# Kernel tuning notes

Measured on AMD Instinct MI355X. Metric: run time of the kernel, lower is better.

The kernel has to match this reference:

```python
import jax, jax.numpy as jnp
import numpy as np

NUM_LAYERS, E, H = 4, 256, 8
HD = E // H
EPS = 1e-5


def _layer_norm(x, g, b):
    m = jnp.mean(x, axis=-1, keepdims=True)
    v = jnp.mean((x - m) ** 2, axis=-1, keepdims=True)
    return (x - m) / jnp.sqrt(v + EPS) * g + b


def _embed_rotary(x, pos):
    # x: [B, L, E], pos: [B, L, E, 2] (cos, sin)
    x2 = jnp.stack([-x[..., 1::2], x[..., ::2]], axis=-1).reshape(x.shape)
    return x * pos[..., 0] + x2 * pos[..., 1]


def setup_inputs() -> dict:
    key = jax.random.key(0)
    ks = jax.random.split(key, 16)
    Lq, B, Lkv = 512, 4, 4096
    s = 0.02
    return {
        "query": jax.random.normal(ks[0], (Lq, B, E), jnp.float32),
        "value": jax.random.normal(ks[1], (Lkv, B, E), jnp.float32),
        "query_pos": jax.random.normal(ks[2], (B, Lq, E, 2), jnp.float32),
        "value_pos": jax.random.normal(ks[3], (B, Lkv, E, 2), jnp.float32),
        "Wqkv": jax.random.normal(ks[4], (NUM_LAYERS, 3 * E, E), jnp.float32) * s,
        "bqkv": jnp.zeros((NUM_LAYERS, 3 * E), jnp.float32),
        "Wo": jax.random.normal(ks[5], (NUM_LAYERS, E, E), jnp.float32) * s,
        "bo": jnp.zeros((NUM_LAYERS, E), jnp.float32),
        "ln1_g": jnp.ones((NUM_LAYERS, E), jnp.float32),
        "ln1_b": jnp.zeros((NUM_LAYERS, E), jnp.float32),
        "W1": jax.random.normal(ks[6], (NUM_LAYERS, E, E), jnp.float32) * s,
        "b1": jnp.zeros((NUM_LAYERS, E), jnp.float32),
        "W2": jax.random.normal(ks[7], (NUM_LAYERS, E, E), jnp.float32) * s,
        "b2": jnp.zeros((NUM_LAYERS, E), jnp.float32),
        "ln2_g": jnp.ones((NUM_LAYERS, E), jnp.float32),
        "ln2_b": jnp.zeros((NUM_LAYERS, E), jnp.float32),
    }


def reference(query, value, query_pos, value_pos, Wqkv, bqkv, Wo, bo,
              ln1_g, ln1_b, W1, b1, W2, b2, ln2_g, ln2_b):
    Lq, B, _ = query.shape
    Lkv = value.shape[0]
    scale = HD ** -0.5

    def step(q_in, p):
        Wqkv_l, bqkv_l, Wo_l, bo_l, g1, be1, W1_l, b1_l, W2_l, b2_l, g2, be2 = p
        Wq, Wk, Wv = jnp.split(Wqkv_l, 3, axis=0)
        bq, bk, bv = jnp.split(bqkv_l, 3, axis=0)
        q = (q_in @ Wq.T + bq) * scale              # [Lq, B, E] (scaled as torch MHA)
        k = value @ Wk.T + bk                        # [Lkv, B, E]
        v = value @ Wv.T + bv
        qb = _embed_rotary(q.swapaxes(0, 1), query_pos)   # [B, Lq, E]
        kb = _embed_rotary(k.swapaxes(0, 1), value_pos)   # [B, Lkv, E]
        vb = v.swapaxes(0, 1)
        qh = qb.reshape(B, Lq, H, HD).transpose(0, 2, 1, 3)    # [B, H, Lq, HD]
        kh = kb.reshape(B, Lkv, H, HD).transpose(0, 2, 1, 3)
        vh = vb.reshape(B, Lkv, H, HD).transpose(0, 2, 1, 3)
        attn = jax.nn.softmax(jnp.einsum('bhqd,bhkd->bhqk', qh, kh), axis=-1)
        o = jnp.einsum('bhqk,bhkd->bhqd', attn, vh)            # [B, H, Lq, HD]
        o = o.transpose(0, 2, 1, 3).reshape(B, Lq, E).swapaxes(0, 1)  # [Lq, B, E]
        x = _layer_norm(q_in + o @ Wo_l.T + bo_l, g1, be1)
        ff = jax.nn.relu(x @ W1_l.T + b1_l) @ W2_l.T + b2_l
        y = _layer_norm(x + ff, g2, be2)
        return y, y

    params = (Wqkv, bqkv, Wo, bo, ln1_g, ln1_b, W1, b1, W2, b2, ln2_g, ln2_b)
    _, ys = jax.lax.scan(step, query, params)
    return ys  # [num_layers, Lq, B, E] — stacked per-layer outputs
```

## Files before the change

kernel.cpp:

```cpp
#include <hip/hip_runtime.h>
#include <hip/hip_bf16.h>

typedef __attribute__((ext_vector_type(8))) short short8;
typedef __attribute__((ext_vector_type(4))) float float4v;
typedef __attribute__((ext_vector_type(4))) unsigned short ushort4v;

#define LQ 512
#define NB 4
#define LKV 4096
#define E 256
#define NH 8
#define HD 32
#define NLAYER 4
#define QSCALE 0.17677669529663687f
#define SPLITS 4
#define KSPAN (LKV / SPLITS)
#define QT 128
#define CK 128

__device__ __forceinline__ unsigned short f2bf(float f) {
    union { float f; unsigned int i; } x; x.f = f;
    unsigned int r = x.i + 0x7fffu + ((x.i >> 16) & 1u);
    return (unsigned short)(r >> 16);
}
__device__ __forceinline__ unsigned int pack2(float a, float b) {
    union { float f; unsigned int i; } xa, xb; xa.f = a; xb.f = b;
    unsigned int ra = xa.i + 0x7fffu + ((xa.i >> 16) & 1u);
    unsigned int rb = xb.i + 0x7fffu + ((xb.i >> 16) & 1u);
    return (ra >> 16) | (rb & 0xffff0000u);
}
__device__ __forceinline__ unsigned int pack2_rtz(float a, float b) {
    union { float f; unsigned int i; } xa, xb; xa.f = a; xb.f = b;
    return __builtin_amdgcn_perm(xb.i, xa.i, 0x07060302u);
}
__device__ __forceinline__ float bf2f(unsigned short u) {
    union { unsigned int i; float f; } x; x.i = ((unsigned int)u) << 16; return x.f;
}
__device__ __forceinline__ float4v mfma16(short8 a, short8 b, float4v c) {
    return __builtin_amdgcn_mfma_f32_16x16x32_bf16(a, b, c, 0, 0, 0);
}

__global__ void pack_k(const float* __restrict__ in, unsigned short* __restrict__ out) {
    long i = ((long)blockIdx.x * 256 + threadIdx.x) * 8;
    float4 a = *(const float4*)&in[i];
    float4 b = *(const float4*)&in[i + 4];
    uint4 v;
    v.x = pack2(a.x, a.y); v.y = pack2(a.z, a.w);
    v.z = pack2(b.x, b.y); v.w = pack2(b.z, b.w);
    *(uint4*)&out[i] = v;
}

__global__ void init_cur(const float* __restrict__ q, float* __restrict__ cur,
                         unsigned short* __restrict__ cur_bf) {
    int i = blockIdx.x * 256 + threadIdx.x;
    float v = q[i];
    cur[i] = v;
    cur_bf[i] = f2bf(v);
}

__global__ __launch_bounds__(256) void gemm_k(
        const unsigned short* __restrict__ A, const unsigned short* __restrict__ W,
        const float* __restrict__ bias, unsigned short* __restrict__ out_bf) {
    __shared__ unsigned short sA[32 * 264];
    __shared__ unsigned short sB[64 * 264];
    const int t = threadIdx.x;
    const int lane = t & 63, wave = t >> 6, quad = lane >> 4, lid = lane & 15;
    const int row0 = blockIdx.x * 32, col0 = blockIdx.y * 64;
    {
        int r = t >> 3, ks = (t & 7) * 32;
        const unsigned short* ap = A + (long)(row0 + r) * E + ks;
#pragma unroll
        for (int i = 0; i < 4; i++)
            *(uint4*)&sA[r * 264 + ks + i * 8] = *(const uint4*)(ap + i * 8);
    }
    {
        int r = t >> 2, ks = (t & 3) * 64;
        const unsigned short* wp = W + (long)(col0 + r) * E + ks;
#pragma unroll
        for (int i = 0; i < 8; i++)
            *(uint4*)&sB[r * 264 + ks + i * 8] = *(const uint4*)(wp + i * 8);
    }
    __syncthreads();
    float4v acc[2];
    acc[0] = (float4v){0.f, 0.f, 0.f, 0.f};
    acc[1] = (float4v){0.f, 0.f, 0.f, 0.f};
#pragma unroll
    for (int k0 = 0; k0 < E; k0 += 32) {
        short8 bf = *(const short8*)&sB[(wave * 16 + lid) * 264 + k0 + quad * 8];
        short8 af0 = *(const short8*)&sA[(lid) * 264 + k0 + quad * 8];
        short8 af1 = *(const short8*)&sA[(16 + lid) * 264 + k0 + quad * 8];
        acc[0] = mfma16(af0, bf, acc[0]);
        acc[1] = mfma16(af1, bf, acc[1]);
    }
#pragma unroll
    for (int mt = 0; mt < 2; mt++)
#pragma unroll
        for (int r = 0; r < 4; r++) {
            int grow = row0 + mt * 16 + quad * 4 + r;
            int gcol = col0 + wave * 16 + lid;
            float v = fmaxf(acc[mt][r] + bias[gcol], 0.f);
            out_bf[(long)grow * E + gcol] = f2bf(v);
        }
}

template <int COMBINE, int OUT2>
__global__ __launch_bounds__(256) void gemm_ln(
        const unsigned short* __restrict__ A,
        const float* __restrict__ Opart, const float* __restrict__ lp,
        const unsigned short* __restrict__ W, const float* __restrict__ bias,
        const float* __restrict__ res, const float* __restrict__ g,
        const float* __restrict__ bvec, float* __restrict__ outf,
        unsigned short* __restrict__ out_bf, float* __restrict__ outf2) {
    __shared__ unsigned short sA[16 * 264];
    __shared__ float lnS[4][16];
    __shared__ float lnQ[4][16];
    const int t = threadIdx.x;
    const int lane = t & 63, wave = t >> 6, quad = lane >> 4, lid = lane & 15;
    const int row0 = blockIdx.x * 16;
    {
        const int r = t >> 4, cseg = t & 15;
        if (COMBINE) {
            const int grow = row0 + r;
            const int seq = grow >> 2, b = grow & 3;
            const int h = cseg >> 1, dd = (cseg & 1) * 16;
            const int bh = b * 8 + h;
            float L = 0.f;
            float av[16];
#pragma unroll
            for (int j = 0; j < 16; j++) av[j] = 0.f;
#pragma unroll
            for (int s = 0; s < SPLITS; s++) {
                long rbase = (long)(s * 32 + bh) * 512 + seq;
                L += lp[rbase];
#pragma unroll
                for (int jj = 0; jj < 4; jj++) {
                    float4 p = *(const float4*)&Opart[rbase * 32 + dd + jj * 4];
                    av[jj * 4 + 0] += p.x; av[jj * 4 + 1] += p.y;
                    av[jj * 4 + 2] += p.z; av[jj * 4 + 3] += p.w;
                }
            }
            float inv = 1.f / L;
            uint4 u0, u1;
            u0.x = pack2(av[0] * inv, av[1] * inv);   u0.y = pack2(av[2] * inv, av[3] * inv);
            u0.z = pack2(av[4] * inv, av[5] * inv);   u0.w = pack2(av[6] * inv, av[7] * inv);
            u1.x = pack2(av[8] * inv, av[9] * inv);   u1.y = pack2(av[10] * inv, av[11] * inv);
            u1.z = pack2(av[12] * inv, av[13] * inv); u1.w = pack2(av[14] * inv, av[15] * inv);
            *(uint4*)&sA[r * 264 + cseg * 16] = u0;
            *(uint4*)&sA[r * 264 + cseg * 16 + 8] = u1;
        } else {
            const unsigned short* ap = A + (long)(row0 + r) * E + cseg * 16;
            *(uint4*)&sA[r * 264 + cseg * 16] = *(const uint4*)ap;
            *(uint4*)&sA[r * 264 + cseg * 16 + 8] = *(const uint4*)(ap + 8);
        }
    }
    __syncthreads();
    float4v acc[4];
#pragma unroll
    for (int nf = 0; nf < 4; nf++) acc[nf] = (float4v){0.f, 0.f, 0.f, 0.f};
#pragma unroll
    for (int k0 = 0; k0 < E; k0 += 32) {
        short8 af = *(const short8*)&sA[lid * 264 + k0 + quad * 8];
#pragma unroll
        for (int nf = 0; nf < 4; nf++) {
            short8 bf = *(const short8*)(W + (long)(wave * 64 + nf * 16 + lid) * E + k0 + quad * 8);
            acc[nf] = mfma16(af, bf, acc[nf]);
        }
    }
    float v[4][4];
    float sr[4], qr_[4];
#pragma unroll
    for (int r = 0; r < 4; r++) { sr[r] = 0.f; qr_[r] = 0.f; }
#pragma unroll
    for (int nf = 0; nf < 4; nf++) {
        int col = wave * 64 + nf * 16 + lid;
        float bcol = bias[col];
#pragma unroll
        for (int r = 0; r < 4; r++) {
            int grow = row0 + quad * 4 + r;
            float val = acc[nf][r] + bcol + res[(long)grow * E + col];
            v[nf][r] = val;
            sr[r] += val;
            qr_[r] += val * val;
        }
    }
#pragma unroll
    for (int r = 0; r < 4; r++) {
#pragma unroll
        for (int d = 1; d < 16; d <<= 1) {
            sr[r] += __shfl_xor(sr[r], d);
            qr_[r] += __shfl_xor(qr_[r], d);
        }
    }
    if (lid == 0) {
#pragma unroll
        for (int r = 0; r < 4; r++) {
            lnS[wave][quad * 4 + r] = sr[r];
            lnQ[wave][quad * 4 + r] = qr_[r];
        }
    }
    __syncthreads();
    float mean[4], rstd[4];
#pragma unroll
    for (int r = 0; r < 4; r++) {
        int row = quad * 4 + r;
        float S = lnS[0][row] + lnS[1][row] + lnS[2][row] + lnS[3][row];
        float Q = lnQ[0][row] + lnQ[1][row] + lnQ[2][row] + lnQ[3][row];
        float mu = S * (1.f / 256.f);
        float var = Q * (1.f / 256.f) - mu * mu;
        mean[r] = mu;
        rstd[r] = rsqrtf(var + 1e-5f);
    }
#pragma unroll
    for (int nf = 0; nf < 4; nf++) {
        int col = wave * 64 + nf * 16 + lid;
        float gc = g[col], bc = bvec[col];
#pragma unroll
        for (int r = 0; r < 4; r++) {
            int grow = row0 + quad * 4 + r;
            float xo = (v[nf][r] - mean[r]) * rstd[r] * gc + bc;
            outf[(long)grow * E + col] = xo;
            out_bf[(long)grow * E + col] = f2bf(xo);
            if (OUT2) outf2[(long)grow * E + col] = xo;
        }
    }
}

__global__ __launch_bounds__(256) void qkv_q(
        const unsigned short* __restrict__ A, const unsigned short* __restrict__ W,
        const float* __restrict__ bias, const unsigned short* __restrict__ pos,
        unsigned short* __restrict__ qout) {
    __shared__ unsigned short sA[32 * 40];
    __shared__ unsigned short sB[64 * 40];
    const int t = threadIdx.x;
    const int lane = t & 63, wave = t >> 6, quad = lane >> 4, lid = lane & 15;
    const int row0 = blockIdx.x * 32, col0 = blockIdx.y * 64;
    const int sr = t >> 2, sk = (t & 3) * 8;
    const unsigned short* ap = A + (long)(row0 + sr) * E + sk;
    const unsigned short* wp = W + (long)(col0 + sr) * E + sk;
    uint4 av, bv;
    if (t < 128) av = *(const uint4*)ap;
    bv = *(const uint4*)wp;
    float4v acc[2];
    acc[0] = (float4v){0.f, 0.f, 0.f, 0.f};
    acc[1] = (float4v){0.f, 0.f, 0.f, 0.f};
#pragma unroll
    for (int ki = 0; ki < 8; ki++) {
        __syncthreads();
        if (t < 128) *(uint4*)&sA[sr * 40 + sk] = av;
        *(uint4*)&sB[sr * 40 + sk] = bv;
        __syncthreads();
        if (ki < 7) {
            if (t < 128) av = *(const uint4*)(ap + (ki + 1) * 32);
            bv = *(const uint4*)(wp + (ki + 1) * 32);
        }
        short8 af0 = *(const short8*)&sA[lid * 40 + quad * 8];
        short8 af1 = *(const short8*)&sA[(16 + lid) * 40 + quad * 8];
        short8 bf = *(const short8*)&sB[(wave * 16 + lid) * 40 + quad * 8];
        acc[0] = mfma16(af0, bf, acc[0]);
        acc[1] = mfma16(af1, bf, acc[1]);
    }
#pragma unroll
    for (int mt = 0; mt < 2; mt++)
#pragma unroll
        for (int r = 0; r < 4; r++) {
            int grow = row0 + mt * 16 + quad * 4 + r;
            int gcol = col0 + wave * 16 + lid;
            float v = (acc[mt][r] + bias[gcol]) * QSCALE;
            int seq = grow >> 2, b = grow & 3;
            int c = gcol;
            unsigned int cs = *(const unsigned int*)&pos[(((long)b * LQ + seq) * E + c) * 2];
            float cv = bf2f((unsigned short)cs), sv = bf2f((unsigned short)(cs >> 16));
            float p = __shfl_xor(v, 1);
            float x2 = (c & 1) ? p : -p;
            float rv = v * cv + x2 * sv;
            qout[(((long)b * NH + (c >> 5)) * LQ + seq) * HD + (c & 31)] = f2bf(rv);
        }
}

__global__ __launch_bounds__(256) void qkv_kv(
        const unsigned short* __restrict__ A, const unsigned short* __restrict__ Wall,
        const float* __restrict__ ball, const unsigned short* __restrict__ pos,
        unsigned short* __restrict__ kall, unsigned short* __restrict__ vtall) {
    const int layer = blockIdx.z;
    const unsigned short* W = Wall + (long)layer * 768 * 256 + 256 * 256;
    const float* bias = ball + (long)layer * 768 + 256;
    unsigned short* kout = kall + (long)layer * 4194304;
    unsigned short* vtout = vtall + (long)layer * 4194304;
    __shared__ unsigned short sA[64 * 40];
    __shared__ unsigned short sB[64 * 40];
    const int t = threadIdx.x;
    const int lane = t & 63, wave = t >> 6, quad = lane >> 4, lid = lane & 15;
    const int wr = wave >> 1, wc = wave & 1;
    const int row0 = blockIdx.x * 64, col0 = blockIdx.y * 64;
    const int sr = t >> 2, sk = (t & 3) * 8;
    const unsigned short* ap = A + (long)(row0 + sr) * E + sk;
    const unsigned short* wp = W + (long)(col0 + sr) * E + sk;
    uint4 av = *(const uint4*)ap;
    uint4 bv = *(const uint4*)wp;
    float4v acc[2][2];
    for (int i = 0; i < 2; i++) for (int j = 0; j < 2; j++) acc[i][j] = (float4v){0.f, 0.f, 0.f, 0.f};
#pragma unroll
    for (int ki = 0; ki < 8; ki++) {
        __syncthreads();
        *(uint4*)&sA[sr * 40 + sk] = av;
        *(uint4*)&sB[sr * 40 + sk] = bv;
        __syncthreads();
        if (ki < 7) {
            av = *(const uint4*)(ap + (ki + 1) * 32);
            bv = *(const uint4*)(wp + (ki + 1) * 32);
        }
        short8 af0 = *(const short8*)&sA[(wr * 32 + lid) * 40 + quad * 8];
        short8 af1 = *(const short8*)&sA[(wr * 32 + 16 + lid) * 40 + quad * 8];
        short8 bf0 = *(const short8*)&sB[(wc * 32 + lid) * 40 + quad * 8];
        short8 bf1 = *(const short8*)&sB[(wc * 32 + 16 + lid) * 40 + quad * 8];
        acc[0][0] = mfma16(af0, bf0, acc[0][0]);
        acc[0][1] = mfma16(af0, bf1, acc[0][1]);
        acc[1][0] = mfma16(af1, bf0, acc[1][0]);
        acc[1][1] = mfma16(af1, bf1, acc[1][1]);
    }
#pragma unroll
    for (int mt = 0; mt < 2; mt++)
#pragma unroll
        for (int nt = 0; nt < 2; nt++)
#pragma unroll
            for (int r = 0; r < 4; r++) {
                int grow = row0 + wr * 32 + mt * 16 + quad * 4 + r;
                int gcol = col0 + wc * 32 + nt * 16 + lid;
                float v = acc[mt][nt][r] + bias[gcol];
                int seq = grow >> 2, b = grow & 3;
                if (gcol < E) {
                    int c = gcol;
                    unsigned int cs = *(const unsigned int*)&pos[(((long)b * LKV + seq) * E + c) * 2];
                    float cv = bf2f((unsigned short)cs), sv = bf2f((unsigned short)(cs >> 16));
                    float p = __shfl_xor(v, 1);
                    float x2 = (c & 1) ? p : -p;
                    float rv = v * cv + x2 * sv;
                    kout[(((long)b * NH + (c >> 5)) * LKV + seq) * HD + (c & 31)] = f2bf(rv);
                } else {
                    int c = gcol - E;
                    vtout[(((long)b * NH + (c >> 5)) * HD + (c & 31)) * (long)LKV + seq] = f2bf(v);
                }
            }
}

__global__ __launch_bounds__(256) void attn_k(
        const unsigned short* __restrict__ qb, const unsigned short* __restrict__ kb,
        const unsigned short* __restrict__ vtb, float* __restrict__ Opart,
        float* __restrict__ lpart) {
    __shared__ unsigned short sK[CK * 40];
    __shared__ unsigned short sVT[32 * 136];
    __shared__ unsigned short sPT[4 * CK * 36];
    const int t = threadIdx.x;
    const int lane = t & 63, wave = t >> 6, quad = lane >> 4, lid = lane & 15;
    const int qt0 = blockIdx.x * QT;
    const int bh = blockIdx.y;
    const int key0 = blockIdx.z * KSPAN;
    const unsigned short* kbase = kb + (long)bh * LKV * HD;
    const unsigned short* vbase = vtb + (long)bh * HD * LKV;
    short8 aq[2];
#pragma unroll
    for (int mf = 0; mf < 2; mf++)
        aq[mf] = *(const short8*)(qb + ((long)bh * LQ + qt0 + wave * 32 + mf * 16 + lid) * HD + quad * 8);
    float4v o[2][2];
#pragma unroll
    for (int i = 0; i < 2; i++) for (int j = 0; j < 2; j++) o[i][j] = (float4v){0.f, 0.f, 0.f, 0.f};
    float l[8] = {0.f, 0.f, 0.f, 0.f, 0.f, 0.f, 0.f, 0.f};
    const int krow = t >> 1, khalf = (t & 1) * 16;
    const int vrow = t >> 3, vkoff = (t & 7) * 16;
    unsigned short* myPT = &sPT[wave * CK * 36];
    for (int ck = key0; ck < key0 + KSPAN; ck += CK) {
        uint4 kv0 = *(const uint4*)(kbase + (long)(ck + krow) * HD + khalf);
        uint4 kv1 = *(const uint4*)(kbase + (long)(ck + krow) * HD + khalf + 8);
        uint4 vv0 = *(const uint4*)(vbase + (long)vrow * LKV + ck + vkoff);
        uint4 vv1 = *(const uint4*)(vbase + (long)vrow * LKV + ck + vkoff + 8);
        __syncthreads();
        *(uint4*)&sK[krow * 40 + khalf] = kv0;
        *(uint4*)&sK[krow * 40 + khalf + 8] = kv1;
        *(uint4*)&sVT[vrow * 136 + vkoff] = vv0;
        *(uint4*)&sVT[vrow * 136 + vkoff + 8] = vv1;
        __syncthreads();
#pragma unroll
        for (int nf = 0; nf < 8; nf++) {
            short8 bk = *(const short8*)&sK[(nf * 16 + lid) * 40 + quad * 8];
#pragma unroll
            for (int mf = 0; mf < 2; mf++) {
                float4v z = (float4v){0.f, 0.f, 0.f, 0.f};
                float4v s = mfma16(aq[mf], bk, z);
                float e0 = __expf(s[0]), e1 = __expf(s[1]);
                float e2 = __expf(s[2]), e3 = __expf(s[3]);
                l[mf * 4 + 0] += e0; l[mf * 4 + 1] += e1;
                l[mf * 4 + 2] += e2; l[mf * 4 + 3] += e3;
                uint2 pk;
                pk.x = pack2_rtz(e0, e1);
                pk.y = pack2_rtz(e2, e3);
                *(uint2*)&myPT[(nf * 16 + lid) * 36 + mf * 16 + quad * 4] = pk;
            }
        }
#pragma unroll
        for (int kb2 = 0; kb2 < 4; kb2++) {
            short8 bv0 = *(const short8*)&sVT[lid * 136 + kb2 * 32 + quad * 8];
            short8 bv1 = *(const short8*)&sVT[(16 + lid) * 136 + kb2 * 32 + quad * 8];
#pragma unroll
            for (int mf = 0; mf < 2; mf++) {
                short8 ap;
#pragma unroll
                for (int j = 0; j < 8; j++)
                    ap[j] = (short)myPT[(kb2 * 32 + quad * 8 + j) * 36 + mf * 16 + lid];
                o[mf][0] = mfma16(ap, bv0, o[mf][0]);
                o[mf][1] = mfma16(ap, bv1, o[mf][1]);
            }
        }
    }
#pragma unroll
    for (int i = 0; i < 8; i++) {
#pragma unroll
        for (int d = 1; d < 16; d <<= 1) l[i] += __shfl_xor(l[i], d);
    }
#pragma unroll
    for (int mf = 0; mf < 2; mf++)
#pragma unroll
        for (int r = 0; r < 4; r++) {
            long orow = ((long)blockIdx.z * 32 + bh) * LQ + qt0 + wave * 32 + mf * 16 + quad * 4 + r;
            Opart[orow * HD + lid] = o[mf][0][r];
            Opart[orow * HD + 16 + lid] = o[mf][1][r];
            if (lid == 0) lpart[orow] = l[mf * 4 + r];
        }
}

extern "C" void kernel_launch(void* const* d_in, const int* in_sizes, int n_in,
                              void* d_out, int out_size, void* d_ws, size_t ws_size,
                              hipStream_t stream) {
    (void)in_sizes; (void)n_in; (void)out_size; (void)ws_size;
    const float* query = (const float*)d_in[0];
    const float* value = (const float*)d_in[1];
    const float* qpos  = (const float*)d_in[2];
    const float* vpos  = (const float*)d_in[3];
    const float* Wqkv  = (const float*)d_in[4];
    const float* bqkv  = (const float*)d_in[5];
    const float* Wo    = (const float*)d_in[6];
    const float* bo    = (const float*)d_in[7];
    const float* g1    = (const float*)d_in[8];
    const float* be1   = (const float*)d_in[9];
    const float* W1    = (const float*)d_in[10];
    const float* b1    = (const float*)d_in[11];
    const float* W2    = (const float*)d_in[12];
    const float* b2    = (const float*)d_in[13];
    const float* g2    = (const float*)d_in[14];
    const float* be2   = (const float*)d_in[15];
    float* outp = (float*)d_out;

    char* w = (char*)d_ws;
    float*          cur     = (float*)(w + 0);
    unsigned short* cur_bf  = (unsigned short*)(w + (2l  << 20));
    unsigned short* qbuf    = (unsigned short*)(w + (3l  << 20));
    float*          xb      = (float*)(w + (4l  << 20));
    unsigned short* xb_bf   = (unsigned short*)(w + (6l  << 20));
    unsigned short* h1b_bf  = (unsigned short*)(w + (7l  << 20));
    float*          lp      = (float*)(w + (8l  << 20));
    float*          Opart   = (float*)(w + (9l  << 20));
    unsigned short* val_bf  = (unsigned short*)(w + (17l << 20));
    unsigned short* wqkv_bf = (unsigned short*)(w + (25l << 20));
    unsigned short* wo_bf   = (unsigned short*)(w + (27l << 20));
    unsigned short* w1_bf   = (unsigned short*)(w + (28l << 20));
    unsigned short* w2_bf   = (unsigned short*)(w + (29l << 20));
    unsigned short* qpos_bf = (unsigned short*)(w + (30l << 20));
    unsigned short* vpos_bf = (unsigned short*)(w + (32l << 20));
    unsigned short* kbuf    = (unsigned short*)(w + (48l << 20));
    unsigned short* vtb     = (unsigned short*)(w + (80l << 20));

    init_cur<<<2048, 256, 0, stream>>>(query, cur, cur_bf);
    pack_k<<<2048, 256, 0, stream>>>(value, val_bf);
    pack_k<<<384,  256, 0, stream>>>(Wqkv, wqkv_bf);
    pack_k<<<128,  256, 0, stream>>>(Wo, wo_bf);
    pack_k<<<128,  256, 0, stream>>>(W1, w1_bf);
    pack_k<<<128,  256, 0, stream>>>(W2, w2_bf);
    pack_k<<<512,  256, 0, stream>>>(qpos, qpos_bf);
    pack_k<<<4096, 256, 0, stream>>>(vpos, vpos_bf);

    qkv_kv<<<dim3(256, 8, NLAYER), 256, 0, stream>>>(val_bf, wqkv_bf, bqkv, vpos_bf, kbuf, vtb);

    for (int layer = 0; layer < NLAYER; layer++) {
        const unsigned short* Wl = wqkv_bf + (long)layer * 768 * 256;
        const float* bl = bqkv + (long)layer * 768;
        qkv_q<<<dim3(64, 4), 256, 0, stream>>>(cur_bf, Wl, bl, qpos_bf, qbuf);
        attn_k<<<dim3(LQ / QT, 32, SPLITS), 256, 0, stream>>>(
            qbuf, kbuf + (long)layer * 4194304, vtb + (long)layer * 4194304, Opart, lp);
        gemm_ln<1, 0><<<128, 256, 0, stream>>>(
            nullptr, Opart, lp, wo_bf + layer * 65536, bo + layer * 256,
            cur, g1 + layer * 256, be1 + layer * 256, xb, xb_bf, nullptr);
        gemm_k<<<dim3(64, 4), 256, 0, stream>>>(xb_bf, w1_bf + layer * 65536, b1 + layer * 256, h1b_bf);
        gemm_ln<0, 1><<<128, 256, 0, stream>>>(
            h1b_bf, nullptr, nullptr, w2_bf + layer * 65536, b2 + layer * 256,
            xb, g2 + layer * 256, be2 + layer * 256, cur, cur_bf,
            outp + (long)layer * LQ * NB * E);
    }
}
```

Measured before the change: 435.2 us.

## Fuse pack kernels, transpose value layout, stage V^T stores, prefetch attention tiles

```diff
diff --git a/kernel.cpp b/kernel.cpp
--- a/kernel.cpp
+++ b/kernel.cpp
@@ -3,7 +3,6 @@
 
 typedef __attribute__((ext_vector_type(8))) short short8;
 typedef __attribute__((ext_vector_type(4))) float float4v;
-typedef __attribute__((ext_vector_type(4))) unsigned short ushort4v;
 
 #define LQ 512
 #define NB 4
@@ -13,10 +12,12 @@
 #define HD 32
 #define NLAYER 4
 #define QSCALE 0.17677669529663687f
-#define SPLITS 4
+#define SPLITS 8
 #define KSPAN (LKV / SPLITS)
 #define QT 128
 #define CK 128
+
+#define LDS_FENCE() asm volatile("s_waitcnt lgkmcnt(0)" ::: "memory")
 
 __device__ __forceinline__ unsigned short f2bf(float f) {
     union { float f; unsigned int i; } x; x.f = f;
@@ -39,23 +40,57 @@
 __device__ __forceinline__ float4v mfma16(short8 a, short8 b, float4v c) {
     return __builtin_amdgcn_mfma_f32_16x16x32_bf16(a, b, c, 0, 0, 0);
 }
-
-__global__ void pack_k(const float* __restrict__ in, unsigned short* __restrict__ out) {
-    long i = ((long)blockIdx.x * 256 + threadIdx.x) * 8;
-    float4 a = *(const float4*)&in[i];
-    float4 b = *(const float4*)&in[i + 4];
+__device__ __forceinline__ void pack_store8(const float* __restrict__ src,
+                                            unsigned short* __restrict__ dst) {
+    float4 a = *(const float4*)src;
+    float4 b = *(const float4*)(src + 4);
     uint4 v;
     v.x = pack2(a.x, a.y); v.y = pack2(a.z, a.w);
     v.z = pack2(b.x, b.y); v.w = pack2(b.z, b.w);
-    *(uint4*)&out[i] = v;
-}
-
-__global__ void init_cur(const float* __restrict__ q, float* __restrict__ cur,
+    *(uint4*)dst = v;
+}
+
+__global__ void pack_all(const float* __restrict__ value, const float* __restrict__ Wqkv,
+                         const float* __restrict__ Wo, const float* __restrict__ W1,
+                         const float* __restrict__ W2, const float* __restrict__ qpos,
+                         const float* __restrict__ vpos, const float* __restrict__ query,
+                         unsigned short* __restrict__ val_t, unsigned short* __restrict__ wqkv_bf,
+                         unsigned short* __restrict__ wo_bf, unsigned short* __restrict__ w1_bf,
+                         unsigned short* __restrict__ w2_bf, unsigned short* __restrict__ qpos_bf,
+                         unsigned short* __restrict__ vpos_bf, float* __restrict__ cur,
                          unsigned short* __restrict__ cur_bf) {
-    int i = blockIdx.x * 256 + threadIdx.x;
-    float v = q[i];
-    cur[i] = v;
-    cur_bf[i] = f2bf(v);
+    int bid = blockIdx.x;
+    if (bid < 2048) {
+        long idx = ((long)bid * 256 + threadIdx.x) * 8;
+        int ro = (int)(idx >> 8), e = (int)(idx & 255);
+        int ri = ((ro & 4095) << 2) | (ro >> 12);
+        pack_store8(value + (long)ri * 256 + e, val_t + idx);
+        return;
+    }
+    bid -= 2048;
+    if (bid < 384) { long i = ((long)bid * 256 + threadIdx.x) * 8; pack_store8(Wqkv + i, wqkv_bf + i); return; }
+    bid -= 384;
+    if (bid < 128) { long i = ((long)bid * 256 + threadIdx.x) * 8; pack_store8(Wo + i, wo_bf + i); return; }
+    bid -= 128;
+    if (bid < 128) { long i = ((long)bid * 256 + threadIdx.x) * 8; pack_store8(W1 + i, w1_bf + i); return; }
+    bid -= 128;
+    if (bid < 128) { long i = ((long)bid * 256 + threadIdx.x) * 8; pack_store8(W2 + i, w2_bf + i); return; }
+    bid -= 128;
+    if (bid < 512) { long i = ((long)bid * 256 + threadIdx.x) * 8; pack_store8(qpos + i, qpos_bf + i); return; }
+    bid -= 512;
+    if (bid < 4096) { long i = ((long)bid * 256 + threadIdx.x) * 8; pack_store8(vpos + i, vpos_bf + i); return; }
+    bid -= 4096;
+    {
+        long i = ((long)bid * 256 + threadIdx.x) * 8;
+        float4 a = *(const float4*)&query[i];
+        float4 b = *(const float4*)&query[i + 4];
+        *(float4*)&cur[i] = a;
+        *(float4*)&cur[i + 4] = b;
+        uint4 v;
+        v.x = pack2(a.x, a.y); v.y = pack2(a.z, a.w);
+        v.z = pack2(b.x, b.y); v.w = pack2(b.z, b.w);
+        *(uint4*)&cur_bf[i] = v;
+    }
 }
 
 __global__ __launch_bounds__(256) void gemm_k(
@@ -104,7 +139,7 @@
 }
 
 template <int COMBINE, int OUT2>
-__global__ __launch_bounds__(256) void gemm_ln(
+__global__ __launch_bounds__(256, 1) void gemm_ln(
         const unsigned short* __restrict__ A,
         const float* __restrict__ Opart, const float* __restrict__ lp,
         const unsigned short* __restrict__ W, const float* __restrict__ bias,
@@ -286,61 +321,84 @@
     const float* bias = ball + (long)layer * 768 + 256;
     unsigned short* kout = kall + (long)layer * 4194304;
     unsigned short* vtout = vtall + (long)layer * 4194304;
-    __shared__ unsigned short sA[64 * 40];
-    __shared__ unsigned short sB[64 * 40];
+    __shared__ unsigned short sA[64 * 72];
+    __shared__ unsigned short sB[64 * 72];
+    __shared__ unsigned short sT[64 * 72];
     const int t = threadIdx.x;
     const int lane = t & 63, wave = t >> 6, quad = lane >> 4, lid = lane & 15;
     const int wr = wave >> 1, wc = wave & 1;
     const int row0 = blockIdx.x * 64, col0 = blockIdx.y * 64;
-    const int sr = t >> 2, sk = (t & 3) * 8;
-    const unsigned short* ap = A + (long)(row0 + sr) * E + sk;
-    const unsigned short* wp = W + (long)(col0 + sr) * E + sk;
-    uint4 av = *(const uint4*)ap;
-    uint4 bv = *(const uint4*)wp;
+    const int b = row0 >> 12, seq0 = row0 & 4095;
+    const int r = t >> 2, kk = (t & 3) * 16;
+    const unsigned short* apg = A + (long)(row0 + r) * E + kk;
+    const unsigned short* wpg = W + (long)(col0 + r) * E + kk;
+    uint4 a0 = *(const uint4*)apg,        a1 = *(const uint4*)(apg + 8);
+    uint4 b0 = *(const uint4*)wpg,        b1 = *(const uint4*)(wpg + 8);
     float4v acc[2][2];
     for (int i = 0; i < 2; i++) for (int j = 0; j < 2; j++) acc[i][j] = (float4v){0.f, 0.f, 0.f, 0.f};
 #pragma unroll
-    for (int ki = 0; ki < 8; ki++) {
-        __syncthreads();
-        *(uint4*)&sA[sr * 40 + sk] = av;
-        *(uint4*)&sB[sr * 40 + sk] = bv;
-        __syncthreads();
-        if (ki < 7) {
-            av = *(const uint4*)(ap + (ki + 1) * 32);
-            bv = *(const uint4*)(wp + (ki + 1) * 32);
-        }
-        short8 af0 = *(const short8*)&sA[(wr * 32 + lid) * 40 + quad * 8];
-        short8 af1 = *(const short8*)&sA[(wr * 32 + 16 + lid) * 40 + quad * 8];
-        short8 bf0 = *(const short8*)&sB[(wc * 32 + lid) * 40 + quad * 8];
-        short8 bf1 = *(const short8*)&sB[(wc * 32 + 16 + lid) * 40 + quad * 8];
-        acc[0][0] = mfma16(af0, bf0, acc[0][0]);
-        acc[0][1] = mfma16(af0, bf1, acc[0][1]);
-        acc[1][0] = mfma16(af1, bf0, acc[1][0]);
-        acc[1][1] = mfma16(af1, bf1, acc[1][1]);
-    }
-#pragma unroll
-    for (int mt = 0; mt < 2; mt++)
-#pragma unroll
-        for (int nt = 0; nt < 2; nt++)
-#pragma unroll
-            for (int r = 0; r < 4; r++) {
-                int grow = row0 + wr * 32 + mt * 16 + quad * 4 + r;
-                int gcol = col0 + wc * 32 + nt * 16 + lid;
-                float v = acc[mt][nt][r] + bias[gcol];
-                int seq = grow >> 2, b = grow & 3;
-                if (gcol < E) {
-                    int c = gcol;
+    for (int ki = 0; ki < 4; ki++) {
+        __syncthreads();
+        *(uint4*)&sA[r * 72 + kk] = a0; *(uint4*)&sA[r * 72 + kk + 8] = a1;
+        *(uint4*)&sB[r * 72 + kk] = b0; *(uint4*)&sB[r * 72 + kk + 8] = b1;
+        __syncthreads();
+        if (ki < 3) {
+            a0 = *(const uint4*)(apg + (ki + 1) * 64); a1 = *(const uint4*)(apg + (ki + 1) * 64 + 8);
+            b0 = *(const uint4*)(wpg + (ki + 1) * 64); b1 = *(const uint4*)(wpg + (ki + 1) * 64 + 8);
+        }
+#pragma unroll
+        for (int kf = 0; kf < 2; kf++) {
+            const int ko = kf * 32 + quad * 8;
+            short8 af0 = *(const short8*)&sA[(wr * 32 + lid) * 72 + ko];
+            short8 af1 = *(const short8*)&sA[(wr * 32 + 16 + lid) * 72 + ko];
+            short8 bf0 = *(const short8*)&sB[(wc * 32 + lid) * 72 + ko];
+            short8 bf1 = *(const short8*)&sB[(wc * 32 + 16 + lid) * 72 + ko];
+            acc[0][0] = mfma16(af0, bf0, acc[0][0]);
+            acc[0][1] = mfma16(af0, bf1, acc[0][1]);
+            acc[1][0] = mfma16(af1, bf0, acc[1][0]);
+            acc[1][1] = mfma16(af1, bf1, acc[1][1]);
+        }
+    }
+    if (col0 < 256) {
+#pragma unroll
+        for (int mt = 0; mt < 2; mt++)
+#pragma unroll
+            for (int nt = 0; nt < 2; nt++)
+#pragma unroll
+                for (int rr = 0; rr < 4; rr++) {
+                    int m = wr * 32 + mt * 16 + quad * 4 + rr;
+                    int c = col0 + wc * 32 + nt * 16 + lid;
+                    int seq = seq0 + m;
+                    float v = acc[mt][nt][rr] + bias[c];
                     unsigned int cs = *(const unsigned int*)&pos[(((long)b * LKV + seq) * E + c) * 2];
                     float cv = bf2f((unsigned short)cs), sv = bf2f((unsigned short)(cs >> 16));
                     float p = __shfl_xor(v, 1);
                     float x2 = (c & 1) ? p : -p;
                     float rv = v * cv + x2 * sv;
                     kout[(((long)b * NH + (c >> 5)) * LKV + seq) * HD + (c & 31)] = f2bf(rv);
-                } else {
-                    int c = gcol - E;
-                    vtout[(((long)b * NH + (c >> 5)) * HD + (c & 31)) * (long)LKV + seq] = f2bf(v);
                 }
+    } else {
+#pragma unroll
+        for (int mt = 0; mt < 2; mt++)
+#pragma unroll
+            for (int nt = 0; nt < 2; nt++) {
+                int cl = wc * 32 + nt * 16 + lid;
+                int so = wr * 32 + mt * 16 + quad * 4;
+                float bcol = bias[col0 + cl];
+                uint2 pw;
+                pw.x = pack2(acc[mt][nt][0] + bcol, acc[mt][nt][1] + bcol);
+                pw.y = pack2(acc[mt][nt][2] + bcol, acc[mt][nt][3] + bcol);
+                *(uint2*)&sT[cl * 72 + so] = pw;
             }
+        __syncthreads();
+        const int cl = t >> 2, sc = (t & 3) * 16;
+        uint4 u0 = *(const uint4*)&sT[cl * 72 + sc];
+        uint4 u1 = *(const uint4*)&sT[cl * 72 + sc + 8];
+        int cg = (col0 - 256) + cl;
+        unsigned short* dst = vtout + (((long)b * NH + (cg >> 5)) * HD + (cg & 31)) * (long)LKV + seq0 + sc;
+        *(uint4*)dst = u0;
+        *(uint4*)(dst + 8) = u1;
+    }
 }
 
 __global__ __launch_bounds__(256) void attn_k(
@@ -349,7 +407,7 @@
         float* __restrict__ lpart) {
     __shared__ unsigned short sK[CK * 40];
     __shared__ unsigned short sVT[32 * 136];
-    __shared__ unsigned short sPT[4 * CK * 36];
+    __shared__ unsigned short sPT[4 * 64 * 36];
     const int t = threadIdx.x;
     const int lane = t & 63, wave = t >> 6, quad = lane >> 4, lid = lane & 15;
     const int qt0 = blockIdx.x * QT;
@@ -367,48 +425,59 @@
     float l[8] = {0.f, 0.f, 0.f, 0.f, 0.f, 0.f, 0.f, 0.f};
     const int krow = t >> 1, khalf = (t & 1) * 16;
     const int vrow = t >> 3, vkoff = (t & 7) * 16;
-    unsigned short* myPT = &sPT[wave * CK * 36];
+    unsigned short* myPT = &sPT[wave * 64 * 36];
+    uint4 kv0 = *(const uint4*)(kbase + (long)(key0 + krow) * HD + khalf);
+    uint4 kv1 = *(const uint4*)(kbase + (long)(key0 + krow) * HD + khalf + 8);
+    uint4 vv0 = *(const uint4*)(vbase + (long)vrow * LKV + key0 + vkoff);
+    uint4 vv1 = *(const uint4*)(vbase + (long)vrow * LKV + key0 + vkoff + 8);
     for (int ck = key0; ck < key0 + KSPAN; ck += CK) {
-        uint4 kv0 = *(const uint4*)(kbase + (long)(ck + krow) * HD + khalf);
-        uint4 kv1 = *(const uint4*)(kbase + (long)(ck + krow) * HD + khalf + 8);
-        uint4 vv0 = *(const uint4*)(vbase + (long)vrow * LKV + ck + vkoff);
-        uint4 vv1 = *(const uint4*)(vbase + (long)vrow * LKV + ck + vkoff + 8);
         __syncthreads();
         *(uint4*)&sK[krow * 40 + khalf] = kv0;
         *(uint4*)&sK[krow * 40 + khalf + 8] = kv1;
         *(uint4*)&sVT[vrow * 136 + vkoff] = vv0;
         *(uint4*)&sVT[vrow * 136 + vkoff + 8] = vv1;
         __syncthreads();
-#pragma unroll
-        for (int nf = 0; nf < 8; nf++) {
-            short8 bk = *(const short8*)&sK[(nf * 16 + lid) * 40 + quad * 8];
-#pragma unroll
-            for (int mf = 0; mf < 2; mf++) {
-                float4v z = (float4v){0.f, 0.f, 0.f, 0.f};
-                float4v s = mfma16(aq[mf], bk, z);
-                float e0 = __expf(s[0]), e1 = __expf(s[1]);
-                float e2 = __expf(s[2]), e3 = __expf(s[3]);
-                l[mf * 4 + 0] += e0; l[mf * 4 + 1] += e1;
-                l[mf * 4 + 2] += e2; l[mf * 4 + 3] += e3;
-                uint2 pk;
-                pk.x = pack2_rtz(e0, e1);
-                pk.y = pack2_rtz(e2, e3);
-                *(uint2*)&myPT[(nf * 16 + lid) * 36 + mf * 16 + quad * 4] = pk;
+        if (ck + CK < key0 + KSPAN) {
+            kv0 = *(const uint4*)(kbase + (long)(ck + CK + krow) * HD + khalf);
+            kv1 = *(const uint4*)(kbase + (long)(ck + CK + krow) * HD + khalf + 8);
+            vv0 = *(const uint4*)(vbase + (long)vrow * LKV + ck + CK + vkoff);
+            vv1 = *(const uint4*)(vbase + (long)vrow * LKV + ck + CK + vkoff + 8);
+        }
+#pragma unroll
+        for (int half = 0; half < 2; half++) {
+#pragma unroll
+            for (int nf = 0; nf < 4; nf++) {
+                short8 bk = *(const short8*)&sK[(half * 64 + nf * 16 + lid) * 40 + quad * 8];
+#pragma unroll
+                for (int mf = 0; mf < 2; mf++) {
+                    float4v z = (float4v){0.f, 0.f, 0.f, 0.f};
+                    float4v s = mfma16(aq[mf], bk, z);
+                    float e0 = __expf(s[0]), e1 = __expf(s[1]);
+                    float e2 = __expf(s[2]), e3 = __expf(s[3]);
+                    l[mf * 4 + 0] += e0; l[mf * 4 + 1] += e1;
+                    l[mf * 4 + 2] += e2; l[mf * 4 + 3] += e3;
+                    uint2 pk;
+                    pk.x = pack2_rtz(e0, e1);
+                    pk.y = pack2_rtz(e2, e3);
+                    *(uint2*)&myPT[(nf * 16 + lid) * 36 + mf * 16 + quad * 4] = pk;
+                }
             }
-        }
-#pragma unroll
-        for (int kb2 = 0; kb2 < 4; kb2++) {
-            short8 bv0 = *(const short8*)&sVT[lid * 136 + kb2 * 32 + quad * 8];
-            short8 bv1 = *(const short8*)&sVT[(16 + lid) * 136 + kb2 * 32 + quad * 8];
-#pragma unroll
-            for (int mf = 0; mf < 2; mf++) {
-                short8 ap;
-#pragma unroll
-                for (int j = 0; j < 8; j++)
-                    ap[j] = (short)myPT[(kb2 * 32 + quad * 8 + j) * 36 + mf * 16 + lid];
-                o[mf][0] = mfma16(ap, bv0, o[mf][0]);
-                o[mf][1] = mfma16(ap, bv1, o[mf][1]);
+            LDS_FENCE();
+#pragma unroll
+            for (int kb2 = 0; kb2 < 2; kb2++) {
+                short8 bv0 = *(const short8*)&sVT[lid * 136 + half * 64 + kb2 * 32 + quad * 8];
+                short8 bv1 = *(const short8*)&sVT[(16 + lid) * 136 + half * 64 + kb2 * 32 + quad * 8];
+#pragma unroll
+                for (int mf = 0; mf < 2; mf++) {
+                    short8 ap;
+#pragma unroll
+                    for (int j = 0; j < 8; j++)
+                        ap[j] = (short)myPT[(kb2 * 32 + quad * 8 + j) * 36 + mf * 16 + lid];
+                    o[mf][0] = mfma16(ap, bv0, o[mf][0]);
+                    o[mf][1] = mfma16(ap, bv1, o[mf][1]);
+                }
             }
+            LDS_FENCE();
         }
     }
 #pragma unroll
@@ -458,26 +527,21 @@
     unsigned short* h1b_bf  = (unsigned short*)(w + (7l  << 20));
     float*          lp      = (float*)(w + (8l  << 20));
     float*          Opart   = (float*)(w + (9l  << 20));
-    unsigned short* val_bf  = (unsigned short*)(w + (17l << 20));
-    unsigned short* wqkv_bf = (unsigned short*)(w + (25l << 20));
-    unsigned short* wo_bf   = (unsigned short*)(w + (27l << 20));
-    unsigned short* w1_bf   = (unsigned short*)(w + (28l << 20));
-    unsigned short* w2_bf   = (unsigned short*)(w + (29l << 20));
-    unsigned short* qpos_bf = (unsigned short*)(w + (30l << 20));
-    unsigned short* vpos_bf = (unsigned short*)(w + (32l << 20));
-    unsigned short* kbuf    = (unsigned short*)(w + (48l << 20));
-    unsigned short* vtb     = (unsigned short*)(w + (80l << 20));
-
-    init_cur<<<2048, 256, 0, stream>>>(query, cur, cur_bf);
-    pack_k<<<2048, 256, 0, stream>>>(value, val_bf);
-    pack_k<<<384,  256, 0, stream>>>(Wqkv, wqkv_bf);
-    pack_k<<<128,  256, 0, stream>>>(Wo, wo_bf);
-    pack_k<<<128,  256, 0, stream>>>(W1, w1_bf);
-    pack_k<<<128,  256, 0, stream>>>(W2, w2_bf);
-    pack_k<<<512,  256, 0, stream>>>(qpos, qpos_bf);
-    pack_k<<<4096, 256, 0, stream>>>(vpos, vpos_bf);
-
-    qkv_kv<<<dim3(256, 8, NLAYER), 256, 0, stream>>>(val_bf, wqkv_bf, bqkv, vpos_bf, kbuf, vtb);
+    unsigned short* val_t   = (unsigned short*)(w + (25l << 20));
+    unsigned short* wqkv_bf = (unsigned short*)(w + (33l << 20));
+    unsigned short* wo_bf   = (unsigned short*)(w + (35l << 20));
+    unsigned short* w1_bf   = (unsigned short*)(w + (36l << 20));
+    unsigned short* w2_bf   = (unsigned short*)(w + (37l << 20));
+    unsigned short* qpos_bf = (unsigned short*)(w + (38l << 20));
+    unsigned short* vpos_bf = (unsigned short*)(w + (40l << 20));
+    unsigned short* kbuf    = (unsigned short*)(w + (56l << 20));
+    unsigned short* vtb     = (unsigned short*)(w + (88l << 20));
+
+    pack_all<<<7680, 256, 0, stream>>>(value, Wqkv, Wo, W1, W2, qpos, vpos, query,
+                                       val_t, wqkv_bf, wo_bf, w1_bf, w2_bf, qpos_bf,
+                                       vpos_bf, cur, cur_bf);
+
+    qkv_kv<<<dim3(256, 8, NLAYER), 256, 0, stream>>>(val_t, wqkv_bf, bqkv, vpos_bf, kbuf, vtb);
 
     for (int layer = 0; layer < NLAYER; layer++) {
         const unsigned short* Wl = wqkv_bf + (long)layer * 768 * 256;
```

Result: faster. 379.4 us (-12.8%).
